# Optimization experiments

Hardware: AMD Instinct MI355X
Metric: run time of the kernel (lower is better)

Reference implementation:

```python
import jax, jax.numpy as jnp
import numpy as np

B, T, D, H, E, K = 4, 2048, 1024, 2048, 8, 2
LN_EPS = 1e-5


def setup_inputs() -> dict:
    key = jax.random.key(0)
    ks = jax.random.split(key, 5)
    sc = 0.02  # init scale for weights
    return {
        "x": jax.random.normal(ks[0], (B, T, D), dtype=jnp.float32),
        "gate_W": jax.random.normal(ks[1], (D, E), dtype=jnp.float32) * sc,
        "gate_b": jnp.zeros((E,), dtype=jnp.float32),
        "W1": jax.random.normal(ks[2], (E, D, H), dtype=jnp.float32) * sc,
        "b1": jnp.zeros((E, H), dtype=jnp.float32),
        "W2": jax.random.normal(ks[3], (E, H, D), dtype=jnp.float32) * sc,
        "b2": jnp.zeros((E, D), dtype=jnp.float32),
        "ln_gamma": jnp.ones((D,), dtype=jnp.float32),
        "ln_beta": jnp.zeros((D,), dtype=jnp.float32),
    }


def reference(x, gate_W, gate_b, W1, b1, W2, b2, ln_gamma, ln_beta):
    b, t, d = x.shape
    tokens = x.reshape(b * t, d)                      # [N, D]
    n = tokens.shape[0]

    # --- noisy top-k router (eval mode: no noise) ---
    logits = tokens @ gate_W + gate_b                 # [N, E]
    topk_val, topk_idx = jax.lax.top_k(logits, K)     # [N, K]
    topk_prob = jax.nn.softmax(topk_val, axis=-1)
    gates = jnp.zeros_like(logits).at[jnp.arange(n)[:, None], topk_idx].set(topk_prob)  # [N, E]

    # --- experts: dense-equivalent of gather-MLP-scatter (gates are 0 for unselected) ---
    h = jax.nn.gelu(jnp.einsum('nd,edh->enh', tokens, W1) + b1[:, None, :], approximate=False)  # [E,N,H]
    y = jnp.einsum('enh,ehd->end', h, W2) + b2[:, None, :]                                      # [E,N,D]
    out = jnp.einsum('ne,end->nd', gates, y).reshape(b, t, d)

    # --- residual + layernorm ---
    z = out + x
    mu = jnp.mean(z, axis=-1, keepdims=True)
    var = jnp.var(z, axis=-1, keepdims=True)
    out = (z - mu) * jax.lax.rsqrt(var + LN_EPS) * ln_gamma + ln_beta

    # --- aux losses ---
    route_probs = jax.nn.softmax(logits, axis=-1)     # [N, E]
    importance = route_probs.mean(axis=0)             # [E]
    load = (gates > 0).astype(jnp.float32).mean(axis=0)  # [E]
    balance_loss = E * jnp.sum(importance * load)
    eps = 1e-8
    entropy = -(route_probs * jnp.log(route_probs + eps)).sum(axis=-1).mean()
    utilization_entropy = -(load * jnp.log(load + eps)).sum()
    return out, balance_loss, entropy, utilization_entropy, load, importance
```

## Files before the change

kernel.cpp:

```cpp
#include <hip/hip_runtime.h>
#include <math.h>

#define N_TOK 8192
#define DIM   1024
#define HID   2048
#define NE    8
#define NPAIR (N_TOK * 2)
#define CAPP  (NPAIR + NE * 128)
#define TAIL  (N_TOK * DIM)

typedef __bf16 bf16x8_t __attribute__((ext_vector_type(8)));
typedef float  f32x4_t  __attribute__((ext_vector_type(4)));

__device__ __forceinline__ unsigned short f2bf(float f) {
  union { float f; unsigned u; } v; v.f = f;
  unsigned r = v.u + 0x7fffu + ((v.u >> 16) & 1u);
  return (unsigned short)(r >> 16);
}

__device__ __forceinline__ float bf2f(unsigned short h) {
  union { unsigned u; float f; } v; v.u = ((unsigned)h) << 16;
  return v.f;
}

__device__ __forceinline__ float gelu_exact(float v) {
  return 0.5f * v * (1.f + erff(v * 0.70710678118654752440f));
}

__device__ __forceinline__ void load16_lds(const void* g, void* l) {
  __builtin_amdgcn_global_load_lds(
      (const __attribute__((address_space(1))) unsigned int*)g,
      (__attribute__((address_space(3))) unsigned int*)l, 16, 0, 0);
}


template<int KD, int RR>
__global__ __launch_bounds__(256) void w_to_frag(const float* __restrict__ src,
                                                 unsigned short* __restrict__ dst) {
  constexpr int KD32 = KD / 32;
  int z = blockIdx.z;
  int cl = blockIdx.x * 4 + (threadIdx.x >> 6);
  int lane = threadIdx.x & 63, m16 = lane & 15, q = lane >> 4;
  int rblk = cl / KD32, kblk = cl % KD32;
  int r = rblk * 16 + m16;
  int kb = kblk * 32 + q * 8;
  const float* s = src + (size_t)z * KD * RR + (size_t)kb * RR + r;
  unsigned short t[8];
  #pragma unroll
  for (int j = 0; j < 8; ++j) t[j] = f2bf(s[(size_t)j * RR]);
  *(uint4*)(dst + (size_t)z * KD * RR + (size_t)cl * 512 + lane * 8) = *(uint4*)t;
}

#define R_BLOCKS 128
#define R_TPW    (N_TOK / (R_BLOCKS * 4))
__global__ __launch_bounds__(256) void router_kernel(
    const float* __restrict__ x, const float* __restrict__ gW, const float* __restrict__ gb,
    int* __restrict__ tok_e, float* __restrict__ tok_g,
    int* __restrict__ cnt, float* __restrict__ imp, float* __restrict__ ent_sum) {
  __shared__ int s_cnt[NE];
  __shared__ float s_imp[NE];
  __shared__ float s_ent;
  int tid = threadIdx.x;
  if (tid < NE) { s_cnt[tid] = 0; s_imp[tid] = 0.f; }
  if (tid == 0) s_ent = 0.f;
  __syncthreads();
  int wid = tid >> 6, lane = tid & 63;
  int t0 = (blockIdx.x * 4 + wid) * R_TPW;
  float imp_loc[8] = {0.f, 0.f, 0.f, 0.f, 0.f, 0.f, 0.f, 0.f};
  float ent_loc = 0.f;
  for (int t = 0; t < R_TPW; ++t) {
    int n = t0 + t;
    const float* xr = x + (size_t)n * DIM;
    float p[8] = {0.f, 0.f, 0.f, 0.f, 0.f, 0.f, 0.f, 0.f};
    #pragma unroll
    for (int it = 0; it < DIM / 64; ++it) {
      int d = lane + (it << 6);
      float xv = xr[d];
      const float4* g4 = (const float4*)(gW + (size_t)d * NE);
      float4 a = g4[0], b = g4[1];
      p[0] += xv * a.x; p[1] += xv * a.y; p[2] += xv * a.z; p[3] += xv * a.w;
      p[4] += xv * b.x; p[5] += xv * b.y; p[6] += xv * b.z; p[7] += xv * b.w;
    }
    #pragma unroll
    for (int e = 0; e < 8; ++e)
      for (int o = 32; o > 0; o >>= 1) p[e] += __shfl_down(p[e], o, 64);
    if (lane == 0) {
      float lg[8];
      #pragma unroll
      for (int e = 0; e < 8; ++e) lg[e] = p[e] + gb[e];
      int i0 = 0;
      #pragma unroll
      for (int e = 1; e < 8; ++e) if (lg[e] > lg[i0]) i0 = e;
      int i1 = (i0 == 0) ? 1 : 0;
      #pragma unroll
      for (int e = 0; e < 8; ++e) if (e != i0 && lg[e] > lg[i1]) i1 = e;
      float d1 = expf(lg[i1] - lg[i0]);
      float g0 = 1.f / (1.f + d1);
      float g1 = d1 * g0;
      tok_e[2 * n] = i0; tok_e[2 * n + 1] = i1;
      tok_g[2 * n] = g0; tok_g[2 * n + 1] = g1;
      atomicAdd(&s_cnt[i0], 1);
      atomicAdd(&s_cnt[i1], 1);
      float mx = lg[i0], s = 0.f, pe[8];
      #pragma unroll
      for (int e = 0; e < 8; ++e) { pe[e] = expf(lg[e] - mx); s += pe[e]; }
      float inv = 1.f / s;
      #pragma unroll
      for (int e = 0; e < 8; ++e) {
        float pr = pe[e] * inv;
        imp_loc[e] += pr;
        ent_loc -= pr * logf(pr + 1e-8f);
      }
    }
  }
  if (lane == 0) {
    #pragma unroll
    for (int e = 0; e < 8; ++e) atomicAdd(&s_imp[e], imp_loc[e]);
    atomicAdd(&s_ent, ent_loc);
  }
  __syncthreads();
  const float invN = 1.f / (float)N_TOK;
  if (tid < NE) {
    atomicAdd(&cnt[tid], s_cnt[tid]);
    atomicAdd(&imp[tid], s_imp[tid] * invN);
  }
  if (tid == NE) atomicAdd(ent_sum, s_ent * invN);
}

__global__ void finalize_kernel(const int* __restrict__ cnt, int* __restrict__ poffs,
                                int* __restrict__ cursor, const float* __restrict__ imp,
                                const float* __restrict__ ent_sum, float* __restrict__ out_tail) {
  if (threadIdx.x == 0) {
    int off = 0; float bal = 0.f, util = 0.f;
    for (int e = 0; e < NE; ++e) {
      poffs[e] = off; cursor[e] = off;
      off += ((cnt[e] + 127) >> 7) << 7;
      float ld = (float)cnt[e] * (1.f / (float)N_TOK);
      float im = imp[e];
      out_tail[3 + e] = ld;
      out_tail[11 + e] = im;
      bal += im * ld;
      util -= ld * logf(ld + 1e-8f);
    }
    poffs[NE] = off;
    out_tail[0] = (float)NE * bal;
    out_tail[1] = *ent_sum;
    out_tail[2] = util;
  }
}

__global__ __launch_bounds__(256) void scatter_kernel(
    const int* __restrict__ tok_e, const float* __restrict__ tok_g,
    int* __restrict__ cursor, int* __restrict__ row_token, float* __restrict__ row_gate,
    int* __restrict__ pair_slot) {
  __shared__ int s_cnt[NE], s_base[NE], s_rank[NE];
  int tid = threadIdx.x;
  if (tid < NE) { s_cnt[tid] = 0; s_rank[tid] = 0; }
  __syncthreads();
  int n = blockIdx.x * 256 + tid;
  int e0 = tok_e[2 * n], e1 = tok_e[2 * n + 1];
  atomicAdd(&s_cnt[e0], 1);
  atomicAdd(&s_cnt[e1], 1);
  __syncthreads();
  if (tid < NE) s_base[tid] = atomicAdd(&cursor[tid], s_cnt[tid]);
  __syncthreads();
  int r0 = atomicAdd(&s_rank[e0], 1);
  int s0 = s_base[e0] + r0;
  row_token[s0] = n; row_gate[s0] = tok_g[2 * n]; pair_slot[2 * n] = s0;
  int r1 = atomicAdd(&s_rank[e1], 1);
  int s1 = s_base[e1] + r1;
  row_token[s1] = n; row_gate[s1] = tok_g[2 * n + 1]; pair_slot[2 * n + 1] = s1;
}

__global__ __launch_bounds__(256) void gather_a1(
    const float* __restrict__ x, const int* __restrict__ row_token,
    const int* __restrict__ cnt, const int* __restrict__ poffs,
    unsigned short* __restrict__ Ab1) {
  int e = blockIdx.z;
  int base = poffs[e];
  int pcnt = poffs[e + 1] - base;
  int nch = (pcnt >> 4) * 32;
  int cl = blockIdx.x * 4 + (threadIdx.x >> 6);
  if (cl >= nch) return;
  int lane = threadIdx.x & 63, m16 = lane & 15, q = lane >> 4;
  int rblk = cl >> 5, kblk = cl & 31;
  int sl = rblk * 16 + m16;
  int slot = base + sl;
  int tok = (sl < cnt[e]) ? row_token[slot] : 0;
  int k = kblk * 32 + q * 8;
  const float4* sp = (const float4*)(x + (size_t)tok * DIM + k);
  float4 v0 = sp[0], v1 = sp[1];
  unsigned short t[8] = {f2bf(v0.x), f2bf(v0.y), f2bf(v0.z), f2bf(v0.w),
                         f2bf(v1.x), f2bf(v1.y), f2bf(v1.z), f2bf(v1.w)};
  *(uint4*)(Ab1 + ((size_t)(slot >> 4) * 32 + kblk) * 512 + lane * 8) = *(uint4*)t;
}

#define GEMM_BLOCKS 1024

__device__ __forceinline__ int xcd_swz(int bid) {
  return (bid & 7) * (GEMM_BLOCKS >> 3) + (bid >> 3);
}

__global__ __launch_bounds__(256, 4) void expert_gemm1(
    const unsigned short* __restrict__ Ab1,
    const unsigned short* __restrict__ W1f,
    const float* __restrict__ b1,
    const int* __restrict__ poffs,
    unsigned short* __restrict__ He) {
  __shared__ __align__(16) unsigned short As[8192], Bs[8192];
  __shared__ int s_po[NE + 1];
  int tid = threadIdx.x, wid = tid >> 6, lane = tid & 63;
  if (tid <= NE) s_po[tid] = poffs[tid];
  __syncthreads();
  int nt = (s_po[NE] >> 7) << 4;
  int m16 = lane & 15, q = lane >> 4;
  int wr = (wid & 1) << 6, wc = (wid >> 1) << 6;
  int ra = wr >> 4, rc = wc >> 4;
  unsigned short* lA = As + wid * 4 * 512;
  unsigned short* lB = Bs + wid * 4 * 512;
  f32x4_t zero4 = {0.f, 0.f, 0.f, 0.f};
  int bid0 = xcd_swz(blockIdx.x);

  for (int tile = bid0; tile < nt; tile += GEMM_BLOCKS) {
    int rt = tile >> 4, ct = tile & 15;
    int col0 = ct << 7;
    int row0 = rt << 7;
    int e = 0;
    while (e + 1 < NE && s_po[e + 1] <= row0) ++e;
    const unsigned short* Ag = Ab1 + ((size_t)((rt << 3) + wid * 2) * 32) * 512 + lane * 8;
    const unsigned short* Bg = W1f + (size_t)e * HID * DIM
                             + ((size_t)((col0 >> 4) + wid * 2) * 32) * 512 + lane * 8;
    f32x4_t acc[4][4];
    #pragma unroll
    for (int i = 0; i < 4; ++i)
      #pragma unroll
      for (int j = 0; j < 4; ++j) acc[i][j] = zero4;

    for (int k0 = 0; k0 < DIM; k0 += 64) {
      int kc = (k0 >> 5) * 512;
      load16_lds(Ag + kc,                  lA);
      load16_lds(Ag + kc + 512,            lA + 512);
      load16_lds(Ag + kc + 32 * 512,       lA + 1024);
      load16_lds(Ag + kc + 32 * 512 + 512, lA + 1536);
      load16_lds(Bg + kc,                  lB);
      load16_lds(Bg + kc + 512,            lB + 512);
      load16_lds(Bg + kc + 32 * 512,       lB + 1024);
      load16_lds(Bg + kc + 32 * 512 + 512, lB + 1536);
      __syncthreads();
      #pragma unroll
      for (int ks = 0; ks < 2; ++ks) {
        bf16x8_t a[4], b[4];
        #pragma unroll
        for (int i = 0; i < 4; ++i) {
          a[i] = *(const bf16x8_t*)&As[((ra + i) * 2 + ks) * 512 + lane * 8];
          b[i] = *(const bf16x8_t*)&Bs[((rc + i) * 2 + ks) * 512 + lane * 8];
        }
        #pragma unroll
        for (int i = 0; i < 4; ++i)
          #pragma unroll
          for (int j = 0; j < 4; ++j)
            acc[i][j] = __builtin_amdgcn_mfma_f32_16x16x32_bf16(a[i], b[j], acc[i][j], 0, 0, 0);
      }
      __syncthreads();
    }

    const float* b1e = b1 + (size_t)e * HID;
    int sb = rt << 3;
    #pragma unroll
    for (int i = 0; i < 4; ++i) {
      size_t sblk = (size_t)(sb + ra + i);
      #pragma unroll
      for (int rr = 0; rr < 4; ++rr) {
        int s15 = q * 4 + rr;
        #pragma unroll
        for (int j = 0; j < 4; ++j) {
          int col = col0 + wc + j * 16 + m16;
          float v = acc[i][j][rr] + b1e[col];
          size_t off = (sblk * 64 + (col >> 5)) * 512 + (((col >> 3) & 3) * 16 + s15) * 8 + (col & 7);
          He[off] = f2bf(gelu_exact(v));
        }
      }
    }
  }
}

__global__ __launch_bounds__(256, 4) void expert_gemm2(
    const unsigned short* __restrict__ He,
    const unsigned short* __restrict__ W2f,
    const int* __restrict__ poffs,
    unsigned short* __restrict__ yb) {
  __shared__ __align__(16) unsigned short As[8192], Bs[8192];
  __shared__ int s_po[NE + 1];
  int tid = threadIdx.x, wid = tid >> 6, lane = tid & 63;
  if (tid <= NE) s_po[tid] = poffs[tid];
  __syncthreads();
  int nt = (s_po[NE] >> 7) << 3;
  int m16 = lane & 15, q = lane >> 4;
  int wr = (wid & 1) << 6, wc = (wid >> 1) << 6;
  int ra = wr >> 4, rc = wc >> 4;
  unsigned short* lA = As + wid * 4 * 512;
  unsigned short* lB = Bs + wid * 4 * 512;
  f32x4_t zero4 = {0.f, 0.f, 0.f, 0.f};
  int bid0 = xcd_swz(blockIdx.x);

  for (int tile = bid0; tile < nt; tile += GEMM_BLOCKS) {
    int rt = tile >> 3, ct = tile & 7;
    int row0 = rt << 7;
    int col0 = ct << 7;
    int e = 0;
    while (e + 1 < NE && s_po[e + 1] <= row0) ++e;
    const unsigned short* Ag = He + ((size_t)((rt << 3) + wid * 2) * 64) * 512 + lane * 8;
    const unsigned short* Bg = W2f + (size_t)e * DIM * HID
                             + ((size_t)((col0 >> 4) + wid * 2) * 64) * 512 + lane * 8;
    f32x4_t acc[4][4];
    #pragma unroll
    for (int i = 0; i < 4; ++i)
      #pragma unroll
      for (int j = 0; j < 4; ++j) acc[i][j] = zero4;

    for (int k0 = 0; k0 < HID; k0 += 64) {
      int kc = (k0 >> 5) * 512;
      load16_lds(Ag + kc,                  lA);
      load16_lds(Ag + kc + 512,            lA + 512);
      load16_lds(Ag + kc + 64 * 512,       lA + 1024);
      load16_lds(Ag + kc + 64 * 512 + 512, lA + 1536);
      load16_lds(Bg + kc,                  lB);
      load16_lds(Bg + kc + 512,            lB + 512);
      load16_lds(Bg + kc + 64 * 512,       lB + 1024);
      load16_lds(Bg + kc + 64 * 512 + 512, lB + 1536);
      __syncthreads();
      #pragma unroll
      for (int ks = 0; ks < 2; ++ks) {
        bf16x8_t a[4], b[4];
        #pragma unroll
        for (int i = 0; i < 4; ++i) {
          a[i] = *(const bf16x8_t*)&As[((ra + i) * 2 + ks) * 512 + lane * 8];
          b[i] = *(const bf16x8_t*)&Bs[((rc + i) * 2 + ks) * 512 + lane * 8];
        }
        #pragma unroll
        for (int i = 0; i < 4; ++i)
          #pragma unroll
          for (int j = 0; j < 4; ++j)
            acc[i][j] = __builtin_amdgcn_mfma_f32_16x16x32_bf16(a[i], b[j], acc[i][j], 0, 0, 0);
      }
      __syncthreads();
    }

    #pragma unroll
    for (int i = 0; i < 4; ++i) {
      #pragma unroll
      for (int rr = 0; rr < 4; ++rr) {
        size_t slot = (size_t)(row0 + wr + i * 16 + q * 4 + rr);
        #pragma unroll
        for (int j = 0; j < 4; ++j) {
          int col = col0 + wc + j * 16 + m16;
          yb[slot * DIM + col] = f2bf(acc[i][j][rr]);
        }
      }
    }
  }
}

__global__ __launch_bounds__(256) void ln_kernel(
    const float* __restrict__ x, const unsigned short* __restrict__ yb,
    const int* __restrict__ tok_e, const float* __restrict__ tok_g,
    const int* __restrict__ pair_slot, const float* __restrict__ b2,
    const float* __restrict__ gamma, const float* __restrict__ beta,
    float* __restrict__ out) {
  int n = blockIdx.x, tid = threadIdx.x;
  int e0 = tok_e[2 * n], e1 = tok_e[2 * n + 1];
  float g0 = tok_g[2 * n], g1 = tok_g[2 * n + 1];
  size_t s0 = (size_t)pair_slot[2 * n], s1 = (size_t)pair_slot[2 * n + 1];
  const float* xr = x + (size_t)n * DIM;
  const unsigned short* y0 = yb + s0 * DIM;
  const unsigned short* y1 = yb + s1 * DIM;
  const float* b2e0 = b2 + (size_t)e0 * DIM;
  const float* b2e1 = b2 + (size_t)e1 * DIM;
  float z[4], s = 0.f, s2 = 0.f;
  #pragma unroll
  for (int jj = 0; jj < 4; ++jj) {
    int d = tid + (jj << 8);
    float v = xr[d] + g0 * (bf2f(y0[d]) + b2e0[d]) + g1 * (bf2f(y1[d]) + b2e1[d]);
    z[jj] = v; s += v; s2 += v * v;
  }
  for (int o = 32; o > 0; o >>= 1) { s += __shfl_down(s, o, 64); s2 += __shfl_down(s2, o, 64); }
  __shared__ float rs[4], rs2[4];
  int wid = tid >> 6, lane = tid & 63;
  if (lane == 0) { rs[wid] = s; rs2[wid] = s2; }
  __syncthreads();
  float ts = rs[0] + rs[1] + rs[2] + rs[3];
  float ts2 = rs2[0] + rs2[1] + rs2[2] + rs2[3];
  float mu = ts * (1.f / DIM);
  float var = ts2 * (1.f / DIM) - mu * mu;
  float rstd = rsqrtf(var + 1e-5f);
  float* orow = out + (size_t)n * DIM;
  #pragma unroll
  for (int jj = 0; jj < 4; ++jj) {
    int d = tid + (jj << 8);
    orow[d] = (z[jj] - mu) * rstd * gamma[d] + beta[d];
  }
}

extern "C" void kernel_launch(void* const* d_in, const int* in_sizes, int n_in,
                              void* d_out, int out_size, void* d_ws, size_t ws_size,
                              hipStream_t stream) {
  const float* x     = (const float*)d_in[0];
  const float* gW    = (const float*)d_in[1];
  const float* gb    = (const float*)d_in[2];
  const float* W1    = (const float*)d_in[3];
  const float* b1    = (const float*)d_in[4];
  const float* W2    = (const float*)d_in[5];
  const float* b2    = (const float*)d_in[6];
  const float* gamma = (const float*)d_in[7];
  const float* beta  = (const float*)d_in[8];
  float* out = (float*)d_out;

  char* w = (char*)d_ws;
  unsigned short* W1f = (unsigned short*)w; w += (size_t)NE * HID * DIM * 2;
  unsigned short* W2f = (unsigned short*)w; w += (size_t)NE * DIM * HID * 2;
  unsigned short* He  = (unsigned short*)w; w += (size_t)CAPP * HID * 2;
  unsigned short* AbY = (unsigned short*)w; w += (size_t)CAPP * DIM * 2;
  int*   row_token    = (int*)w;            w += (size_t)CAPP * 4;
  float* row_gate     = (float*)w;          w += (size_t)CAPP * 4;
  int*   tok_e        = (int*)w;            w += (size_t)NPAIR * 4;
  float* tok_g        = (float*)w;          w += (size_t)NPAIR * 4;
  int*   pair_slot    = (int*)w;            w += (size_t)NPAIR * 4;
  float* imp          = (float*)w;
  float* ent_sum      = imp + 8;
  int*   cntp         = (int*)(imp + 16);
  int*   cursor       = cntp + 8;
  int*   poffs        = cursor + 8;

  unsigned short* Ab1 = AbY;
  unsigned short* yb  = AbY;

  hipMemsetAsync(imp, 0, 256, stream);

  w_to_frag<DIM, HID><<<dim3(1024, 1, NE), 256, 0, stream>>>(W1, W1f);
  w_to_frag<HID, DIM><<<dim3(1024, 1, NE), 256, 0, stream>>>(W2, W2f);
  router_kernel<<<R_BLOCKS, 256, 0, stream>>>(x, gW, gb, tok_e, tok_g, cntp, imp, ent_sum);
  finalize_kernel<<<1, 64, 0, stream>>>(cntp, poffs, cursor, imp, ent_sum, out + TAIL);
  scatter_kernel<<<N_TOK / 256, 256, 0, stream>>>(tok_e, tok_g, cursor, row_token, row_gate, pair_slot);
  gather_a1<<<dim3(4096, 1, NE), 256, 0, stream>>>(x, row_token, cntp, poffs, Ab1);
  expert_gemm1<<<GEMM_BLOCKS, 256, 0, stream>>>(Ab1, W1f, b1, poffs, He);
  expert_gemm2<<<GEMM_BLOCKS, 256, 0, stream>>>(He, W2f, poffs, yb);
  ln_kernel<<<N_TOK, 256, 0, stream>>>(x, yb, tok_e, tok_g, pair_slot, b2, gamma, beta, out);
}
```

Before: 479.1 us.

## Switch expert GEMMs to contiguous tile ranges with more resident blocks

Raises the persistent grid from 1024 to 1280 blocks and the occupancy hint from 4 to 5 blocks per CU. Each block now takes a contiguous range of tiles instead of striding through them, which spreads the uneven tile count more evenly and keeps neighbouring tiles, which share weights, on the same XCD. Expert offsets are read into registers and the expert index comes from a branchless count, removing a shared-memory array and a barrier. The higher occupancy target may force register spilling, and the LDS use of 32KB per block may not allow five blocks per CU.

```diff
diff --git a/kernel.cpp b/kernel.cpp
--- a/kernel.cpp
+++ b/kernel.cpp
@@ -195,38 +195,41 @@
   *(uint4*)(Ab1 + ((size_t)(slot >> 4) * 32 + kblk) * 512 + lane * 8) = *(uint4*)t;
 }
 
-#define GEMM_BLOCKS 1024
+#define GEMM_BLOCKS 1280
 
 __device__ __forceinline__ int xcd_swz(int bid) {
   return (bid & 7) * (GEMM_BLOCKS >> 3) + (bid >> 3);
 }
 
-__global__ __launch_bounds__(256, 4) void expert_gemm1(
+__global__ __launch_bounds__(256, 5) void expert_gemm1(
     const unsigned short* __restrict__ Ab1,
     const unsigned short* __restrict__ W1f,
     const float* __restrict__ b1,
     const int* __restrict__ poffs,
     unsigned short* __restrict__ He) {
   __shared__ __align__(16) unsigned short As[8192], Bs[8192];
-  __shared__ int s_po[NE + 1];
   int tid = threadIdx.x, wid = tid >> 6, lane = tid & 63;
-  if (tid <= NE) s_po[tid] = poffs[tid];
-  __syncthreads();
-  int nt = (s_po[NE] >> 7) << 4;
+  int po[NE + 1];
+  #pragma unroll
+  for (int i = 0; i <= NE; ++i) po[i] = poffs[i];
+  int nt = (po[NE] >> 7) << 4;
   int m16 = lane & 15, q = lane >> 4;
   int wr = (wid & 1) << 6, wc = (wid >> 1) << 6;
   int ra = wr >> 4, rc = wc >> 4;
   unsigned short* lA = As + wid * 4 * 512;
   unsigned short* lB = Bs + wid * 4 * 512;
   f32x4_t zero4 = {0.f, 0.f, 0.f, 0.f};
-  int bid0 = xcd_swz(blockIdx.x);
-
-  for (int tile = bid0; tile < nt; tile += GEMM_BLOCKS) {
+  int swz = xcd_swz(blockIdx.x);
+  int lo = (int)(((long long)swz * nt) / GEMM_BLOCKS);
+  int hi = (int)(((long long)(swz + 1) * nt) / GEMM_BLOCKS);
+
+  for (int tile = lo; tile < hi; ++tile) {
     int rt = tile >> 4, ct = tile & 15;
     int col0 = ct << 7;
     int row0 = rt << 7;
     int e = 0;
-    while (e + 1 < NE && s_po[e + 1] <= row0) ++e;
+    #pragma unroll
+    for (int k = 1; k < NE; ++k) e += (po[k] <= row0) ? 1 : 0;
     const unsigned short* Ag = Ab1 + ((size_t)((rt << 3) + wid * 2) * 32) * 512 + lane * 8;
     const unsigned short* Bg = W1f + (size_t)e * HID * DIM
                              + ((size_t)((col0 >> 4) + wid * 2) * 32) * 512 + lane * 8;
@@ -284,31 +287,34 @@
   }
 }
 
-__global__ __launch_bounds__(256, 4) void expert_gemm2(
+__global__ __launch_bounds__(256, 5) void expert_gemm2(
     const unsigned short* __restrict__ He,
     const unsigned short* __restrict__ W2f,
     const int* __restrict__ poffs,
     unsigned short* __restrict__ yb) {
   __shared__ __align__(16) unsigned short As[8192], Bs[8192];
-  __shared__ int s_po[NE + 1];
   int tid = threadIdx.x, wid = tid >> 6, lane = tid & 63;
-  if (tid <= NE) s_po[tid] = poffs[tid];
-  __syncthreads();
-  int nt = (s_po[NE] >> 7) << 3;
+  int po[NE + 1];
+  #pragma unroll
+  for (int i = 0; i <= NE; ++i) po[i] = poffs[i];
+  int nt = (po[NE] >> 7) << 3;
   int m16 = lane & 15, q = lane >> 4;
   int wr = (wid & 1) << 6, wc = (wid >> 1) << 6;
   int ra = wr >> 4, rc = wc >> 4;
   unsigned short* lA = As + wid * 4 * 512;
   unsigned short* lB = Bs + wid * 4 * 512;
   f32x4_t zero4 = {0.f, 0.f, 0.f, 0.f};
-  int bid0 = xcd_swz(blockIdx.x);
-
-  for (int tile = bid0; tile < nt; tile += GEMM_BLOCKS) {
+  int swz = xcd_swz(blockIdx.x);
+  int lo = (int)(((long long)swz * nt) / GEMM_BLOCKS);
+  int hi = (int)(((long long)(swz + 1) * nt) / GEMM_BLOCKS);
+
+  for (int tile = lo; tile < hi; ++tile) {
     int rt = tile >> 3, ct = tile & 7;
     int row0 = rt << 7;
     int col0 = ct << 7;
     int e = 0;
-    while (e + 1 < NE && s_po[e + 1] <= row0) ++e;
+    #pragma unroll
+    for (int k = 1; k < NE; ++k) e += (po[k] <= row0) ? 1 : 0;
     const unsigned short* Ag = He + ((size_t)((rt << 3) + wid * 2) * 64) * 512 + lane * 8;
     const unsigned short* Bg = W2f + (size_t)e * DIM * HID
                              + ((size_t)((col0 >> 4) + wid * 2) * 64) * 512 + lane * 8;
```

After: 987.5 us. 2.06x slower.

## Fuse expert GEMM1 and GEMM2 into one persistent kernel with per-row-tile ready flags

Applied to the files above, without the earlier changes.

Merges the two expert GEMM kernels into a single launch. Each block takes a contiguous range of work units, where every 128-row tile has 16 GEMM1 column tiles and 8 GEMM2 column tiles. GEMM1 tiles increment an atomic ready counter after writing their GELU output, and GEMM2 tiles spin (with sleep and a guard) until all 16 producers for that row tile are done. The aim is to remove the kernel boundary and let GEMM2 overlap the tail of GEMM1. The cost is spin-waiting that can hold compute units, uneven per-block cost because GEMM2 units have twice the K depth, and reliance on producer blocks being scheduled so waiting blocks do not stall.

```diff
diff --git a/kernel.cpp b/kernel.cpp
--- a/kernel.cpp
+++ b/kernel.cpp
@@ -201,160 +201,158 @@
   return (bid & 7) * (GEMM_BLOCKS >> 3) + (bid >> 3);
 }
 
-__global__ __launch_bounds__(256, 4) void expert_gemm1(
+__global__ __launch_bounds__(256, 4) void expert_mlp(
     const unsigned short* __restrict__ Ab1,
     const unsigned short* __restrict__ W1f,
     const float* __restrict__ b1,
+    const unsigned short* __restrict__ W2f,
     const int* __restrict__ poffs,
-    unsigned short* __restrict__ He) {
+    unsigned short* __restrict__ He,
+    unsigned short* __restrict__ yb,
+    int* __restrict__ rdy) {
   __shared__ __align__(16) unsigned short As[8192], Bs[8192];
-  __shared__ int s_po[NE + 1];
   int tid = threadIdx.x, wid = tid >> 6, lane = tid & 63;
-  if (tid <= NE) s_po[tid] = poffs[tid];
-  __syncthreads();
-  int nt = (s_po[NE] >> 7) << 4;
   int m16 = lane & 15, q = lane >> 4;
   int wr = (wid & 1) << 6, wc = (wid >> 1) << 6;
   int ra = wr >> 4, rc = wc >> 4;
   unsigned short* lA = As + wid * 4 * 512;
   unsigned short* lB = Bs + wid * 4 * 512;
   f32x4_t zero4 = {0.f, 0.f, 0.f, 0.f};
-  int bid0 = xcd_swz(blockIdx.x);
-
-  for (int tile = bid0; tile < nt; tile += GEMM_BLOCKS) {
-    int rt = tile >> 4, ct = tile & 15;
-    int col0 = ct << 7;
+  int nrt = poffs[NE] >> 7;
+  int W = nrt << 5;
+  int swz = xcd_swz(blockIdx.x);
+  int lo = (int)(((long long)swz * W) / GEMM_BLOCKS);
+  int hi = (int)(((long long)(swz + 1) * W) / GEMM_BLOCKS);
+
+  for (int u = lo; u < hi; ++u) {
+    int rt = u >> 5, r = u & 31;
     int row0 = rt << 7;
     int e = 0;
-    while (e + 1 < NE && s_po[e + 1] <= row0) ++e;
-    const unsigned short* Ag = Ab1 + ((size_t)((rt << 3) + wid * 2) * 32) * 512 + lane * 8;
-    const unsigned short* Bg = W1f + (size_t)e * HID * DIM
-                             + ((size_t)((col0 >> 4) + wid * 2) * 32) * 512 + lane * 8;
-    f32x4_t acc[4][4];
     #pragma unroll
-    for (int i = 0; i < 4; ++i)
-      #pragma unroll
-      for (int j = 0; j < 4; ++j) acc[i][j] = zero4;
-
-    for (int k0 = 0; k0 < DIM; k0 += 64) {
-      int kc = (k0 >> 5) * 512;
-      load16_lds(Ag + kc,                  lA);
-      load16_lds(Ag + kc + 512,            lA + 512);
-      load16_lds(Ag + kc + 32 * 512,       lA + 1024);
-      load16_lds(Ag + kc + 32 * 512 + 512, lA + 1536);
-      load16_lds(Bg + kc,                  lB);
-      load16_lds(Bg + kc + 512,            lB + 512);
-      load16_lds(Bg + kc + 32 * 512,       lB + 1024);
-      load16_lds(Bg + kc + 32 * 512 + 512, lB + 1536);
+    for (int k = 1; k < NE; ++k) e += (poffs[k] <= row0) ? 1 : 0;
+
+    if (r < 16) {
+      int col0 = r << 7;
+      const unsigned short* Ag = Ab1 + ((size_t)((rt << 3) + wid * 2) * 32) * 512 + lane * 8;
+      const unsigned short* Bg = W1f + (size_t)e * HID * DIM
+                               + ((size_t)((col0 >> 4) + wid * 2) * 32) * 512 + lane * 8;
+      f32x4_t acc[4][4];
+      #pragma unroll
+      for (int i = 0; i < 4; ++i)
+        #pragma unroll
+        for (int j = 0; j < 4; ++j) acc[i][j] = zero4;
+
+      for (int k0 = 0; k0 < DIM; k0 += 64) {
+        int kc = (k0 >> 5) * 512;
+        load16_lds(Ag + kc,                  lA);
+        load16_lds(Ag + kc + 512,            lA + 512);
+        load16_lds(Ag + kc + 32 * 512,       lA + 1024);
+        load16_lds(Ag + kc + 32 * 512 + 512, lA + 1536);
+        load16_lds(Bg + kc,                  lB);
+        load16_lds(Bg + kc + 512,            lB + 512);
+        load16_lds(Bg + kc + 32 * 512,       lB + 1024);
+        load16_lds(Bg + kc + 32 * 512 + 512, lB + 1536);
+        __syncthreads();
+        #pragma unroll
+        for (int ks = 0; ks < 2; ++ks) {
+          bf16x8_t a[4], b[4];
+          #pragma unroll
+          for (int i = 0; i < 4; ++i) {
+            a[i] = *(const bf16x8_t*)&As[((ra + i) * 2 + ks) * 512 + lane * 8];
+            b[i] = *(const bf16x8_t*)&Bs[((rc + i) * 2 + ks) * 512 + lane * 8];
+          }
+          #pragma unroll
+          for (int i = 0; i < 4; ++i)
+            #pragma unroll
+            for (int j = 0; j < 4; ++j)
+              acc[i][j] = __builtin_amdgcn_mfma_f32_16x16x32_bf16(a[i], b[j], acc[i][j], 0, 0, 0);
+        }
+        __syncthreads();
+      }
+
+      const float* b1e = b1 + (size_t)e * HID;
+      int sb = rt << 3;
+      #pragma unroll
+      for (int i = 0; i < 4; ++i) {
+        size_t sblk = (size_t)(sb + ra + i);
+        #pragma unroll
+        for (int rr = 0; rr < 4; ++rr) {
+          int s15 = q * 4 + rr;
+          #pragma unroll
+          for (int j = 0; j < 4; ++j) {
+            int col = col0 + wc + j * 16 + m16;
+            float v = acc[i][j][rr] + b1e[col];
+            size_t off = (sblk * 64 + (col >> 5)) * 512 + (((col >> 3) & 3) * 16 + s15) * 8 + (col & 7);
+            He[off] = f2bf(gelu_exact(v));
+          }
+        }
+      }
+      asm volatile("s_waitcnt vmcnt(0)" ::: "memory");
       __syncthreads();
-      #pragma unroll
-      for (int ks = 0; ks < 2; ++ks) {
-        bf16x8_t a[4], b[4];
-        #pragma unroll
-        for (int i = 0; i < 4; ++i) {
-          a[i] = *(const bf16x8_t*)&As[((ra + i) * 2 + ks) * 512 + lane * 8];
-          b[i] = *(const bf16x8_t*)&Bs[((rc + i) * 2 + ks) * 512 + lane * 8];
+      if (tid == 0) {
+        __threadfence();
+        atomicAdd(&rdy[rt], 1);
+      }
+    } else if (!(r & 1)) {
+      int ct = (r - 16) >> 1;
+      int col0 = ct << 7;
+      if (tid == 0) {
+        int guard = 0;
+        while (atomicAdd(&rdy[rt], 0) < 16 && guard < (1 << 22)) {
+          __builtin_amdgcn_s_sleep(8);
+          ++guard;
         }
-        #pragma unroll
-        for (int i = 0; i < 4; ++i)
-          #pragma unroll
-          for (int j = 0; j < 4; ++j)
-            acc[i][j] = __builtin_amdgcn_mfma_f32_16x16x32_bf16(a[i], b[j], acc[i][j], 0, 0, 0);
+        __threadfence();
       }
       __syncthreads();
-    }
-
-    const float* b1e = b1 + (size_t)e * HID;
-    int sb = rt << 3;
-    #pragma unroll
-    for (int i = 0; i < 4; ++i) {
-      size_t sblk = (size_t)(sb + ra + i);
-      #pragma unroll
-      for (int rr = 0; rr < 4; ++rr) {
-        int s15 = q * 4 + rr;
-        #pragma unroll
-        for (int j = 0; j < 4; ++j) {
-          int col = col0 + wc + j * 16 + m16;
-          float v = acc[i][j][rr] + b1e[col];
-          size_t off = (sblk * 64 + (col >> 5)) * 512 + (((col >> 3) & 3) * 16 + s15) * 8 + (col & 7);
-          He[off] = f2bf(gelu_exact(v));
+
+      const unsigned short* Ag = He + ((size_t)((rt << 3) + wid * 2) * 64) * 512 + lane * 8;
+      const unsigned short* Bg = W2f + (size_t)e * DIM * HID
+                               + ((size_t)((col0 >> 4) + wid * 2) * 64) * 512 + lane * 8;
+      f32x4_t acc[4][4];
+      #pragma unroll
+      for (int i = 0; i < 4; ++i)
+        #pragma unroll
+        for (int j = 0; j < 4; ++j) acc[i][j] = zero4;
+
+      for (int k0 = 0; k0 < HID; k0 += 64) {
+        int kc = (k0 >> 5) * 512;
+        load16_lds(Ag + kc,                  lA);
+        load16_lds(Ag + kc + 512,            lA + 512);
+        load16_lds(Ag + kc + 64 * 512,       lA + 1024);
+        load16_lds(Ag + kc + 64 * 512 + 512, lA + 1536);
+        load16_lds(Bg + kc,                  lB);
+        load16_lds(Bg + kc + 512,            lB + 512);
+        load16_lds(Bg + kc + 64 * 512,       lB + 1024);
+        load16_lds(Bg + kc + 64 * 512 + 512, lB + 1536);
+        __syncthreads();
+        #pragma unroll
+        for (int ks = 0; ks < 2; ++ks) {
+          bf16x8_t a[4], b[4];
+          #pragma unroll
+          for (int i = 0; i < 4; ++i) {
+            a[i] = *(const bf16x8_t*)&As[((ra + i) * 2 + ks) * 512 + lane * 8];
+            b[i] = *(const bf16x8_t*)&Bs[((rc + i) * 2 + ks) * 512 + lane * 8];
+          }
+          #pragma unroll
+          for (int i = 0; i < 4; ++i)
+            #pragma unroll
+            for (int j = 0; j < 4; ++j)
+              acc[i][j] = __builtin_amdgcn_mfma_f32_16x16x32_bf16(a[i], b[j], acc[i][j], 0, 0, 0);
         }
-      }
-    }
-  }
-}
-
-__global__ __launch_bounds__(256, 4) void expert_gemm2(
-    const unsigned short* __restrict__ He,
-    const unsigned short* __restrict__ W2f,
-    const int* __restrict__ poffs,
-    unsigned short* __restrict__ yb) {
-  __shared__ __align__(16) unsigned short As[8192], Bs[8192];
-  __shared__ int s_po[NE + 1];
-  int tid = threadIdx.x, wid = tid >> 6, lane = tid & 63;
-  if (tid <= NE) s_po[tid] = poffs[tid];
-  __syncthreads();
-  int nt = (s_po[NE] >> 7) << 3;
-  int m16 = lane & 15, q = lane >> 4;
-  int wr = (wid & 1) << 6, wc = (wid >> 1) << 6;
-  int ra = wr >> 4, rc = wc >> 4;
-  unsigned short* lA = As + wid * 4 * 512;
-  unsigned short* lB = Bs + wid * 4 * 512;
-  f32x4_t zero4 = {0.f, 0.f, 0.f, 0.f};
-  int bid0 = xcd_swz(blockIdx.x);
-
-  for (int tile = bid0; tile < nt; tile += GEMM_BLOCKS) {
-    int rt = tile >> 3, ct = tile & 7;
-    int row0 = rt << 7;
-    int col0 = ct << 7;
-    int e = 0;
-    while (e + 1 < NE && s_po[e + 1] <= row0) ++e;
-    const unsigned short* Ag = He + ((size_t)((rt << 3) + wid * 2) * 64) * 512 + lane * 8;
-    const unsigned short* Bg = W2f + (size_t)e * DIM * HID
-                             + ((size_t)((col0 >> 4) + wid * 2) * 64) * 512 + lane * 8;
-    f32x4_t acc[4][4];
-    #pragma unroll
-    for (int i = 0; i < 4; ++i)
-      #pragma unroll
-      for (int j = 0; j < 4; ++j) acc[i][j] = zero4;
-
-    for (int k0 = 0; k0 < HID; k0 += 64) {
-      int kc = (k0 >> 5) * 512;
-      load16_lds(Ag + kc,                  lA);
-      load16_lds(Ag + kc + 512,            lA + 512);
-      load16_lds(Ag + kc + 64 * 512,       lA + 1024);
-      load16_lds(Ag + kc + 64 * 512 + 512, lA + 1536);
-      load16_lds(Bg + kc,                  lB);
-      load16_lds(Bg + kc + 512,            lB + 512);
-      load16_lds(Bg + kc + 64 * 512,       lB + 1024);
-      load16_lds(Bg + kc + 64 * 512 + 512, lB + 1536);
-      __syncthreads();
-      #pragma unroll
-      for (int ks = 0; ks < 2; ++ks) {
-        bf16x8_t a[4], b[4];
-        #pragma unroll
-        for (int i = 0; i < 4; ++i) {
-          a[i] = *(const bf16x8_t*)&As[((ra + i) * 2 + ks) * 512 + lane * 8];
-          b[i] = *(const bf16x8_t*)&Bs[((rc + i) * 2 + ks) * 512 + lane * 8];
-        }
-        #pragma unroll
-        for (int i = 0; i < 4; ++i)
-          #pragma unroll
-          for (int j = 0; j < 4; ++j)
-            acc[i][j] = __builtin_amdgcn_mfma_f32_16x16x32_bf16(a[i], b[j], acc[i][j], 0, 0, 0);
-      }
-      __syncthreads();
-    }
-
-    #pragma unroll
-    for (int i = 0; i < 4; ++i) {
-      #pragma unroll
-      for (int rr = 0; rr < 4; ++rr) {
-        size_t slot = (size_t)(row0 + wr + i * 16 + q * 4 + rr);
-        #pragma unroll
-        for (int j = 0; j < 4; ++j) {
-          int col = col0 + wc + j * 16 + m16;
-          yb[slot * DIM + col] = f2bf(acc[i][j][rr]);
+        __syncthreads();
+      }
+
+      #pragma unroll
+      for (int i = 0; i < 4; ++i) {
+        #pragma unroll
+        for (int rr = 0; rr < 4; ++rr) {
+          size_t slot = (size_t)(row0 + wr + i * 16 + q * 4 + rr);
+          #pragma unroll
+          for (int j = 0; j < 4; ++j) {
+            int col = col0 + wc + j * 16 + m16;
+            yb[slot * DIM + col] = f2bf(acc[i][j][rr]);
+          }
         }
       }
     }
@@ -430,11 +428,12 @@
   int*   cntp         = (int*)(imp + 16);
   int*   cursor       = cntp + 8;
   int*   poffs        = cursor + 8;
+  int*   rdy          = (int*)(imp + 64);
 
   unsigned short* Ab1 = AbY;
   unsigned short* yb  = AbY;
 
-  hipMemsetAsync(imp, 0, 256, stream);
+  hipMemsetAsync(imp, 0, 1024, stream);
 
   w_to_frag<DIM, HID><<<dim3(1024, 1, NE), 256, 0, stream>>>(W1, W1f);
   w_to_frag<HID, DIM><<<dim3(1024, 1, NE), 256, 0, stream>>>(W2, W2f);
@@ -442,7 +441,6 @@
   finalize_kernel<<<1, 64, 0, stream>>>(cntp, poffs, cursor, imp, ent_sum, out + TAIL);
   scatter_kernel<<<N_TOK / 256, 256, 0, stream>>>(tok_e, tok_g, cursor, row_token, row_gate, pair_slot);
   gather_a1<<<dim3(4096, 1, NE), 256, 0, stream>>>(x, row_token, cntp, poffs, Ab1);
-  expert_gemm1<<<GEMM_BLOCKS, 256, 0, stream>>>(Ab1, W1f, b1, poffs, He);
-  expert_gemm2<<<GEMM_BLOCKS, 256, 0, stream>>>(He, W2f, poffs, yb);
+  expert_mlp<<<GEMM_BLOCKS, 256, 0, stream>>>(Ab1, W1f, b1, W2f, poffs, He, yb, rdy);
   ln_kernel<<<N_TOK, 256, 0, stream>>>(x, yb, tok_e, tok_g, pair_slot, b2, gamma, beta, out);
 }
```

Measured after the change: 1.030 ms. 115% more time.
